# Kernel optimization log

Measured on AMD Instinct MI355X. Metric: run time of the kernel, lower is better.

## Reference

```python
import jax, jax.numpy as jnp
import numpy as np
import math

B, S, D, H, L, V = 2, 2048, 1024, 16, 2, 32000
HD = D // H          # head_dim = 64
FF = 4 * D           # ffn hidden = 4096
NEG_INF = -1e9


def setup_inputs() -> dict:
    key = jax.random.key(0)
    ks = jax.random.split(key, 12)
    w = lambda k, shape: jax.random.normal(k, shape, dtype=jnp.float32) * 0.02
    return {
        "tokens": jax.random.randint(ks[0], (B, S), 0, V),
        "tok_emb": w(ks[1], (V, D)),
        "pos_emb": w(ks[2], (S, D)),
        # torch nn.Linear weights are [out, in]; stacked over layers
        "wq": w(ks[3], (L, D, D)),
        "wk": w(ks[4], (L, D, D)),
        "wv": w(ks[5], (L, D, D)),
        "wo": w(ks[6], (L, D, D)),
        "w1": w(ks[7], (L, FF, D)),
        "w2": w(ks[8], (L, D, FF)),
        "ln1_g": jnp.ones((L, D)), "ln1_b": jnp.zeros((L, D)),
        "ln2_g": jnp.ones((L, D)), "ln2_b": jnp.zeros((L, D)),
        "lnf_g": jnp.ones((D,)), "lnf_b": jnp.zeros((D,)),
        "w_out": w(ks[9], (V, D)),
    }


def _layernorm(x, g, b):
    m = jnp.mean(x, axis=-1, keepdims=True)
    v = jnp.mean(jnp.square(x - m), axis=-1, keepdims=True)
    return (x - m) * jax.lax.rsqrt(v + 1e-5) * g + b


def _transformer(tokens, tok_emb, pos_emb, wq, wk, wv, wo, w1, w2,
                 ln1_g, ln1_b, ln2_g, ln2_b, lnf_g, lnf_b, w_out):
    s = tokens.shape[1]
    # causal additive mask [1,1,S,S]
    mask = jnp.where(jnp.tril(jnp.ones((s, s), dtype=bool)), 0.0, NEG_INF)[None, None]
    h = tok_emb[tokens] + pos_emb[None, :s]
    scale = 1.0 / math.sqrt(HD)
    for l in range(L):
        # pre-norm attention
        a_in = _layernorm(h, ln1_g[l], ln1_b[l])
        q = (a_in @ wq[l].T).reshape(B, s, H, HD)
        k = (a_in @ wk[l].T).reshape(B, s, H, HD)
        v = (a_in @ wv[l].T).reshape(B, s, H, HD)
        scores = jnp.einsum('bqhd,bkhd->bhqk', q, k) * scale + mask
        attn = jax.nn.softmax(scores.astype(jnp.float32), axis=-1).astype(h.dtype)
        o = jnp.einsum('bhqk,bkhd->bqhd', attn, v).reshape(B, s, D)
        h = h + o @ wo[l].T
        # pre-norm ReLU FFN
        f_in = _layernorm(h, ln2_g[l], ln2_b[l])
        h = h + jax.nn.relu(f_in @ w1[l].T) @ w2[l].T
    h = _layernorm(h, lnf_g, lnf_b)
    return h @ w_out.T  # [B,S,V]


def reference(tokens, tok_emb, pos_emb, wq, wk, wv, wo, w1, w2,
              ln1_g, ln1_b, ln2_g, ln2_b, lnf_g, lnf_b, w_out):
    return _transformer(tokens, tok_emb, pos_emb, wq, wk, wv, wo, w1, w2,
                        ln1_g, ln1_b, ln2_g, ln2_b, lnf_g, lnf_b, w_out)
```

## Files before the change

kernel.cpp:

```cpp
#include <hip/hip_runtime.h>

#define Bv 2
#define Sv 2048
#define Dv 1024
#define Hv 16
#define HDv 64
#define FFv 4096
#define Vv 32000

typedef short bf16x8 __attribute__((ext_vector_type(8)));
typedef float f32x4 __attribute__((ext_vector_type(4)));
typedef unsigned short us8 __attribute__((ext_vector_type(8)));
typedef unsigned short us4 __attribute__((ext_vector_type(4)));
typedef unsigned short u16;

__device__ __forceinline__ u16 f2bf(float f) {
  union { float f; unsigned u; } x; x.f = f;
  x.u += 0x7fffu + ((x.u >> 16) & 1u);
  return (u16)(x.u >> 16);
}
__device__ __forceinline__ u16 f2bf_rtz(float f) {
  union { float f; unsigned u; } x; x.f = f;
  return (u16)(x.u >> 16);
}

__device__ __forceinline__ void gld16(const void* g, void* l) {
  __builtin_amdgcn_global_load_lds(
      (const __attribute__((address_space(1))) unsigned*)g,
      (__attribute__((address_space(3))) unsigned*)l, 16, 0, 0);
}

__global__ __launch_bounds__(256) void k_embed(const int* __restrict__ tok,
    const float* __restrict__ te, const float* __restrict__ pe,
    float* __restrict__ h) {
  int row = blockIdx.x;
  int s = row & (Sv - 1);
  int t = tok[row];
  float4 va = ((const float4*)(te + (size_t)t * Dv))[threadIdx.x];
  float4 vb = ((const float4*)(pe + (size_t)s * Dv))[threadIdx.x];
  float4 o;
  o.x = va.x + vb.x; o.y = va.y + vb.y; o.z = va.z + vb.z; o.w = va.w + vb.w;
  ((float4*)(h + (size_t)row * Dv))[threadIdx.x] = o;
}

__global__ __launch_bounds__(256) void k_cvt(const float* __restrict__ x,
    u16* __restrict__ y, int n4) {
  int i = blockIdx.x * 256 + threadIdx.x;
  if (i >= n4) return;
  float4 v = ((const float4*)x)[i];
  us4 o = { f2bf(v.x), f2bf(v.y), f2bf(v.z), f2bf(v.w) };
  ((us4*)y)[i] = o;
}

__global__ __launch_bounds__(256) void k_ln(const float* __restrict__ x,
    const float* __restrict__ g, const float* __restrict__ bb,
    u16* __restrict__ y) {
  int row = blockIdx.x, t = threadIdx.x;
  float4 v = ((const float4*)(x + (size_t)row * Dv))[t];
  float s = v.x + v.y + v.z + v.w;
#pragma unroll
  for (int m = 32; m; m >>= 1) s += __shfl_xor(s, m, 64);
  __shared__ float red[4];
  if ((t & 63) == 0) red[t >> 6] = s;
  __syncthreads();
  float mean = (red[0] + red[1] + red[2] + red[3]) * (1.0f / Dv);
  __syncthreads();
  float dx = v.x - mean, dy = v.y - mean, dz = v.z - mean, dw = v.w - mean;
  float s2 = dx * dx + dy * dy + dz * dz + dw * dw;
#pragma unroll
  for (int m = 32; m; m >>= 1) s2 += __shfl_xor(s2, m, 64);
  if ((t & 63) == 0) red[t >> 6] = s2;
  __syncthreads();
  float var = (red[0] + red[1] + red[2] + red[3]) * (1.0f / Dv);
  float rstd = rsqrtf(var + 1e-5f);
  float4 gg = ((const float4*)g)[t];
  float4 be = ((const float4*)bb)[t];
  us4 o = { f2bf(dx * rstd * gg.x + be.x), f2bf(dy * rstd * gg.y + be.y),
            f2bf(dz * rstd * gg.z + be.z), f2bf(dw * rstd * gg.w + be.w) };
  ((us4*)(y + (size_t)row * Dv))[t] = o;
}

__device__ __forceinline__ void stage32(const u16* __restrict__ g, int ldK,
    u16* lds, int row_base, int kt, int lane) {
  int row = row_base + (lane >> 2);
  int slot = (lane & 3) ^ ((row >> 1) & 3);
  const u16* src = g + (size_t)row * ldK + (kt << 5) + (slot << 3);
  gld16(src, lds + (row_base << 5));
}
__device__ __forceinline__ bf16x8 ldfragA(const u16* lds, int row, int ks) {
  return *(const bf16x8*)((const char*)lds + row * 64 + ((ks ^ ((row >> 1) & 3)) << 4));
}

template <int EPI>
__global__ __launch_bounds__(512, 4) void k_gemm8(const u16* __restrict__ A,
    const u16* __restrict__ Bm, const float* __restrict__ res,
    float* __restrict__ Cf, u16* __restrict__ Cb, int M, int N, int K) {
  __shared__ u16 As[3][128 * 32];
  __shared__ u16 Bs[3][256 * 32];
  int TM = M >> 7, TN = N >> 8, nwg = TM * TN;
  int orig = blockIdx.x;
  int qd = nwg >> 3, rm = nwg & 7, xcd = orig & 7;
  int wg = (xcd < rm ? xcd * (qd + 1) : rm * (qd + 1) + (xcd - rm) * qd) + (orig >> 3);
  int bm = wg % TM, bn = wg / TM;
  int m0 = bm << 7, n0 = bn << 8;
  int lane = threadIdx.x & 63, wid = threadIdx.x >> 6;
  int wr = wid >> 2, wc = wid & 3;
  int NT = K >> 5;
  const u16* Ag = A + (size_t)m0 * K;
  const u16* Bg = Bm + (size_t)n0 * K;
  int frow = lane & 15, ks = lane >> 4;

  f32x4 acc[4][4] = {};
  bf16x8 af[4], bf[4];

#pragma unroll
  for (int tt = 0; tt < 2; tt++) {
    stage32(Ag, K, As[tt], wid * 16, tt, lane);
    stage32(Bg, K, Bs[tt], wid * 32, tt, lane);
    stage32(Bg, K, Bs[tt], wid * 32 + 16, tt, lane);
  }
  asm volatile("s_waitcnt vmcnt(3)" ::: "memory");
  __builtin_amdgcn_s_barrier();

  int p = 0;
  for (int t = 0; t < NT; t++) {
    int q = p + 2 >= 3 ? p - 1 : p + 2;
    if (t + 2 < NT) {
      stage32(Ag, K, As[q], wid * 16, t + 2, lane);
      stage32(Bg, K, Bs[q], wid * 32, t + 2, lane);
      stage32(Bg, K, Bs[q], wid * 32 + 16, t + 2, lane);
    }
    const u16* Ab = As[p];
    const u16* Bb = Bs[p];
#pragma unroll
    for (int f = 0; f < 4; f++) af[f] = ldfragA(Ab, wr * 64 + f * 16 + frow, ks);
#pragma unroll
    for (int n = 0; n < 4; n++) bf[n] = ldfragA(Bb, wc * 64 + n * 16 + frow, ks);
    __builtin_amdgcn_s_setprio(1);
#pragma unroll
    for (int f = 0; f < 4; f++)
#pragma unroll
      for (int n = 0; n < 4; n++)
        acc[f][n] = __builtin_amdgcn_mfma_f32_16x16x32_bf16(af[f], bf[n], acc[f][n], 0, 0, 0);
    __builtin_amdgcn_s_setprio(0);
    if (t + 2 < NT) { asm volatile("s_waitcnt vmcnt(3)" ::: "memory"); }
    else            { asm volatile("s_waitcnt vmcnt(0)" ::: "memory"); }
    __builtin_amdgcn_s_barrier();
    p = p + 1 >= 3 ? 0 : p + 1;
  }

#pragma unroll
  for (int f = 0; f < 4; f++) {
#pragma unroll
    for (int r = 0; r < 4; r++) {
      int row = m0 + wr * 64 + f * 16 + (lane >> 4) * 4 + r;
#pragma unroll
      for (int n = 0; n < 4; n++) {
        int col = n0 + wc * 64 + n * 16 + frow;
        float val = acc[f][n][r];
        size_t idx = (size_t)row * N + col;
        if constexpr (EPI == 1) { Cf[idx] = val + res[idx]; }
        else if constexpr (EPI == 0) { __builtin_nontemporal_store(val, &Cf[idx]); }
        else if constexpr (EPI == 2) { Cb[idx] = f2bf(val); }
        else { Cb[idx] = f2bf(fmaxf(val, 0.0f)); }
      }
    }
  }
}

template <int EPI>
__global__ __launch_bounds__(256, 4) void k_gemmn(const u16* __restrict__ A,
    const u16* __restrict__ Bm, const float* __restrict__ res,
    float* __restrict__ Cf, u16* __restrict__ Cb, int M, int N, int K) {
  __shared__ u16 As[3][64 * 32];
  __shared__ u16 Bs[3][128 * 32];
  int TM = M >> 6, TN = N >> 7, nwg = TM * TN;
  int orig = blockIdx.x;
  int qd = nwg >> 3, rm = nwg & 7, xcd = orig & 7;
  int wg = (xcd < rm ? xcd * (qd + 1) : rm * (qd + 1) + (xcd - rm) * qd) + (orig >> 3);
  int bm = wg % TM, bn = wg / TM;
  int m0 = bm << 6, n0 = bn << 7;
  int lane = threadIdx.x & 63, wid = threadIdx.x >> 6;
  int wr = wid >> 1, wc = wid & 1;
  int NT = K >> 5;
  const u16* Ag = A + (size_t)m0 * K;
  const u16* Bg = Bm + (size_t)n0 * K;
  int frow = lane & 15, ks = lane >> 4;

  f32x4 acc[2][4] = {};
  bf16x8 af[2], bf[4];

#pragma unroll
  for (int tt = 0; tt < 2; tt++) {
    stage32(Ag, K, As[tt], wid * 16, tt, lane);
    stage32(Bg, K, Bs[tt], wid * 32, tt, lane);
    stage32(Bg, K, Bs[tt], wid * 32 + 16, tt, lane);
  }
  asm volatile("s_waitcnt vmcnt(3)" ::: "memory");
  __builtin_amdgcn_s_barrier();

  int p = 0;
  for (int t = 0; t < NT; t++) {
    int q = p + 2 >= 3 ? p - 1 : p + 2;
    if (t + 2 < NT) {
      stage32(Ag, K, As[q], wid * 16, t + 2, lane);
      stage32(Bg, K, Bs[q], wid * 32, t + 2, lane);
      stage32(Bg, K, Bs[q], wid * 32 + 16, t + 2, lane);
    }
    const u16* Ab = As[p];
    const u16* Bb = Bs[p];
#pragma unroll
    for (int f = 0; f < 2; f++) af[f] = ldfragA(Ab, wr * 32 + f * 16 + frow, ks);
#pragma unroll
    for (int n = 0; n < 4; n++) bf[n] = ldfragA(Bb, wc * 64 + n * 16 + frow, ks);
    __builtin_amdgcn_s_setprio(1);
#pragma unroll
    for (int f = 0; f < 2; f++)
#pragma unroll
      for (int n = 0; n < 4; n++)
        acc[f][n] = __builtin_amdgcn_mfma_f32_16x16x32_bf16(af[f], bf[n], acc[f][n], 0, 0, 0);
    __builtin_amdgcn_s_setprio(0);
    if (t + 2 < NT) { asm volatile("s_waitcnt vmcnt(3)" ::: "memory"); }
    else            { asm volatile("s_waitcnt vmcnt(0)" ::: "memory"); }
    __builtin_amdgcn_s_barrier();
    p = p + 1 >= 3 ? 0 : p + 1;
  }

#pragma unroll
  for (int f = 0; f < 2; f++) {
#pragma unroll
    for (int r = 0; r < 4; r++) {
      int row = m0 + wr * 32 + f * 16 + (lane >> 4) * 4 + r;
#pragma unroll
      for (int n = 0; n < 4; n++) {
        int col = n0 + wc * 64 + n * 16 + frow;
        float val = acc[f][n][r];
        size_t idx = (size_t)row * N + col;
        if constexpr (EPI == 1) { Cf[idx] = val + res[idx]; }
        else if constexpr (EPI == 0) { __builtin_nontemporal_store(val, &Cf[idx]); }
        else if constexpr (EPI == 2) { Cb[idx] = f2bf(val); }
        else { Cb[idx] = f2bf(fmaxf(val, 0.0f)); }
      }
    }
  }
}

__global__ __launch_bounds__(256) void k_transpose(const u16* __restrict__ v,
    u16* __restrict__ vt, int stride) {
  int st = blockIdx.x & 31;
  int bh = blockIdx.x >> 5;
  int b = bh >> 4, hh = bh & 15;
  __shared__ u16 tile[64][72];
  int t = threadIdx.x;
  int rr = t >> 3, cc = (t & 7) << 3;
#pragma unroll
  for (int it = 0; it < 2; it++) {
    int r = rr + it * 32;
    us8 val = *(const us8*)(v + (size_t)(b * Sv + st * 64 + r) * stride + hh * HDv + cc);
    *(us8*)&tile[r][cc] = val;
  }
  __syncthreads();
#pragma unroll
  for (int it = 0; it < 2; it++) {
    int d = rr + it * 32;
    us8 val;
#pragma unroll
    for (int j = 0; j < 8; j++) val[j] = tile[cc + j][d];
    *(us8*)(vt + ((size_t)bh * HDv + d) * Sv + st * 64 + cc) = val;
  }
}

__global__ __launch_bounds__(64) void k_attn(const u16* __restrict__ qg,
    const u16* __restrict__ kg, const u16* __restrict__ vt,
    u16* __restrict__ og) {
  int bid = blockIdx.x;
  int qt = 15 - (bid >> 7);
  int bh = (bid >> 2) & 31;
  int strip = bid & 3;
  int b = bh >> 4, hh = bh & 15;
  int lane = threadIdx.x;
  int q0 = qt * 128 + strip * 32;
  __shared__ u16 plds[32 * 40];
  const int QS = 3 * Dv;
  const float sc2 = 0.18033688f;
  int qcol = lane & 15, g = lane >> 4;

  bf16x8 onesf;
#pragma unroll
  for (int j = 0; j < 8; j++) onesf[j] = (short)0x3F80;

  bf16x8 qf[2][2];
#pragma unroll
  for (int fm = 0; fm < 2; fm++)
#pragma unroll
    for (int dh = 0; dh < 2; dh++)
      qf[fm][dh] = *(const bf16x8*)(qg + (size_t)(b * Sv + q0 + fm * 16 + qcol) * QS
                                    + hh * HDv + dh * 32 + g * 8);

  f32x4 oacc[2][4] = {};
  f32x4 sacc[2] = {};
  int nfull = q0 >> 5;

  for (int kt = 0; kt <= nfull; kt++) {
    int k0 = kt * 32;
    bool diag = (kt == nfull);
    bf16x8 kf[2][2];
#pragma unroll
    for (int kn = 0; kn < 2; kn++)
#pragma unroll
      for (int dh = 0; dh < 2; dh++)
        kf[kn][dh] = *(const bf16x8*)(kg + (size_t)(b * Sv + k0 + kn * 16 + qcol) * QS
                                      + hh * HDv + dh * 32 + g * 8);
    f32x4 sa[2][2] = {};
#pragma unroll
    for (int dh = 0; dh < 2; dh++)
#pragma unroll
      for (int fm = 0; fm < 2; fm++)
#pragma unroll
        for (int kn = 0; kn < 2; kn++)
          sa[fm][kn] = __builtin_amdgcn_mfma_f32_16x16x32_bf16(kf[kn][dh], qf[fm][dh], sa[fm][kn], 0, 0, 0);

#pragma unroll
    for (int fm = 0; fm < 2; fm++) {
      int qrow = fm * 16 + qcol;
      float pv[2][4];
#pragma unroll
      for (int kn = 0; kn < 2; kn++)
#pragma unroll
        for (int r = 0; r < 4; r++) {
          float e = exp2f(sa[fm][kn][r] * sc2);
          if (diag && (kn * 16 + g * 4 + r) > qrow) e = 0.0f;
          pv[kn][r] = e;
        }
#pragma unroll
      for (int kn = 0; kn < 2; kn++) {
        us4 pk = { f2bf_rtz(pv[kn][0]), f2bf_rtz(pv[kn][1]),
                   f2bf_rtz(pv[kn][2]), f2bf_rtz(pv[kn][3]) };
        *(us4*)(plds + (fm * 16 + qcol) * 40 + kn * 16 + g * 4) = pk;
      }
    }
    bf16x8 pf[2];
#pragma unroll
    for (int fm = 0; fm < 2; fm++)
      pf[fm] = *(const bf16x8*)(plds + (fm * 16 + qcol) * 40 + g * 8);
    bf16x8 vf[4];
#pragma unroll
    for (int dn = 0; dn < 4; dn++)
      vf[dn] = *(const bf16x8*)(vt + ((size_t)bh * HDv + dn * 16 + qcol) * Sv
                                + k0 + g * 8);
#pragma unroll
    for (int fm = 0; fm < 2; fm++) {
      sacc[fm] = __builtin_amdgcn_mfma_f32_16x16x32_bf16(pf[fm], onesf, sacc[fm], 0, 0, 0);
#pragma unroll
      for (int dn = 0; dn < 4; dn++)
        oacc[fm][dn] = __builtin_amdgcn_mfma_f32_16x16x32_bf16(pf[fm], vf[dn], oacc[fm][dn], 0, 0, 0);
    }
  }

#pragma unroll
  for (int fm = 0; fm < 2; fm++)
#pragma unroll
    for (int r = 0; r < 4; r++) {
      float li = 1.0f / sacc[fm][r];
      int row = q0 + fm * 16 + g * 4 + r;
#pragma unroll
      for (int dn = 0; dn < 4; dn++)
        og[(size_t)(b * Sv + row) * Dv + hh * HDv + dn * 16 + qcol] =
            f2bf(oacc[fm][dn][r] * li);
    }
}

extern "C" void kernel_launch(void* const* d_in, const int* in_sizes, int n_in,
                              void* d_out, int out_size, void* d_ws, size_t ws_size,
                              hipStream_t stream) {
  const int*   tok  = (const int*)d_in[0];
  const float* te   = (const float*)d_in[1];
  const float* pe   = (const float*)d_in[2];
  const float* wq   = (const float*)d_in[3];
  const float* wk   = (const float*)d_in[4];
  const float* wvv  = (const float*)d_in[5];
  const float* wo   = (const float*)d_in[6];
  const float* w1   = (const float*)d_in[7];
  const float* w2   = (const float*)d_in[8];
  const float* ln1g = (const float*)d_in[9];
  const float* ln1b = (const float*)d_in[10];
  const float* ln2g = (const float*)d_in[11];
  const float* ln2b = (const float*)d_in[12];
  const float* lnfg = (const float*)d_in[13];
  const float* lnfb = (const float*)d_in[14];
  const float* wout = (const float*)d_in[15];
  float* out = (float*)d_out;

  char* p = (char*)d_ws;
  float* h  = (float*)p; p += (size_t)4096 * 1024 * 4;
  u16* a    = (u16*)p;   p += (size_t)4096 * 1024 * 2;
  u16* qkv  = (u16*)p;   p += (size_t)4096 * 3072 * 2;
  u16* vt   = (u16*)p;   p += (size_t)32 * 64 * 2048 * 2;
  u16* o    = (u16*)p;   p += (size_t)4096 * 1024 * 2;
  u16* f1   = (u16*)p;   p += (size_t)4096 * 4096 * 2;
  u16* wb   = (u16*)p;   p += (size_t)32000 * 1024 * 2;

  const int M = Bv * Sv;

  k_embed<<<M, 256, 0, stream>>>(tok, te, pe, h);
  for (int l = 0; l < 2; l++) {
    k_ln<<<M, 256, 0, stream>>>(h, ln1g + l * Dv, ln1b + l * Dv, a);
    k_cvt<<<1024, 256, 0, stream>>>(wq  + (size_t)l * Dv * Dv, wb,              (Dv * Dv) / 4);
    k_cvt<<<1024, 256, 0, stream>>>(wk  + (size_t)l * Dv * Dv, wb + Dv * Dv,    (Dv * Dv) / 4);
    k_cvt<<<1024, 256, 0, stream>>>(wvv + (size_t)l * Dv * Dv, wb + 2 * Dv * Dv,(Dv * Dv) / 4);
    k_gemm8<2><<<32 * 12, 512, 0, stream>>>(a, wb, nullptr, nullptr, qkv, M, 3 * Dv, Dv);
    k_transpose<<<1024, 256, 0, stream>>>(qkv + 2 * Dv, vt, 3 * Dv);
    k_attn<<<2048, 64, 0, stream>>>(qkv, qkv + Dv, vt, o);
    k_cvt<<<1024, 256, 0, stream>>>(wo + (size_t)l * Dv * Dv, wb, (Dv * Dv) / 4);
    k_gemmn<1><<<64 * 8, 256, 0, stream>>>(o, wb, h, h, nullptr, M, Dv, Dv);
    k_ln<<<M, 256, 0, stream>>>(h, ln2g + l * Dv, ln2b + l * Dv, a);
    k_cvt<<<4096, 256, 0, stream>>>(w1 + (size_t)l * FFv * Dv, wb, (FFv * Dv) / 4);
    k_gemm8<3><<<32 * 16, 512, 0, stream>>>(a, wb, nullptr, nullptr, f1, M, FFv, Dv);
    k_cvt<<<4096, 256, 0, stream>>>(w2 + (size_t)l * Dv * FFv, wb, (Dv * FFv) / 4);
    k_gemmn<1><<<64 * 8, 256, 0, stream>>>(f1, wb, h, h, nullptr, M, Dv, FFv);
  }
  k_ln<<<M, 256, 0, stream>>>(h, lnfg, lnfb, a);
  k_cvt<<<32000, 256, 0, stream>>>(wout, wb, (Vv * Dv) / 4);
  k_gemm8<0><<<32 * 125, 512, 0, stream>>>(a, wb, nullptr, out, nullptr, M, Vv, Dv);
}
```

Measured before the change: 932.0 us.

## Load GEMM B fragments directly from global into registers, merge QKV weight conversions

The GEMM kernels stop staging the weight (B) operand through LDS. Each wave now loads its own B fragments straight from global memory into double-buffered registers one k-tile ahead, while A stays in a three-stage LDS pipeline. This removes B LDS traffic and halves shared memory, but each B load is an uncoalesced 16-byte access per lane, and B data is no longer shared between the waves that need the same columns. Separately, the three Q/K/V weight conversion launches are merged into a single kernel.

```diff
diff --git a/kernel.cpp b/kernel.cpp
--- a/kernel.cpp
+++ b/kernel.cpp
@@ -52,6 +52,18 @@
   ((us4*)y)[i] = o;
 }
 
+__global__ __launch_bounds__(256) void k_cvt3(const float* __restrict__ a,
+    const float* __restrict__ b, const float* __restrict__ c,
+    u16* __restrict__ y, int n4each) {
+  int i = blockIdx.x * 256 + threadIdx.x;
+  int sel = i / n4each;
+  int j = i - sel * n4each;
+  const float* src = sel == 0 ? a : (sel == 1 ? b : c);
+  float4 v = ((const float4*)src)[j];
+  us4 o = { f2bf(v.x), f2bf(v.y), f2bf(v.z), f2bf(v.w) };
+  ((us4*)y)[i] = o;
+}
+
 __global__ __launch_bounds__(256) void k_ln(const float* __restrict__ x,
     const float* __restrict__ g, const float* __restrict__ bb,
     u16* __restrict__ y) {
@@ -91,12 +103,39 @@
   return *(const bf16x8*)((const char*)lds + row * 64 + ((ks ^ ((row >> 1) & 3)) << 4));
 }
 
+#define TILE8(T, CUR, NXT, P)                                                \
+  {                                                                          \
+    if ((T) + 1 < NT) {                                                      \
+      const u16* bp = Bgw + ((T) + 1) * 32;                                  \
+      _Pragma("unroll")                                                      \
+      for (int n = 0; n < 4; n++)                                            \
+        NXT[n] = *(const bf16x8*)(bp + (size_t)n * 16 * K);                  \
+    }                                                                        \
+    if ((T) + 2 < NT)                                                        \
+      stage32(Ag, K, As[(P) + 2 >= 3 ? (P) - 1 : (P) + 2], wid * 16,         \
+              (T) + 2, lane);                                                \
+    _Pragma("unroll")                                                        \
+    for (int f = 0; f < 4; f++)                                              \
+      af[f] = ldfragA(As[P], wr * 64 + f * 16 + frow, ks);                   \
+    __builtin_amdgcn_s_setprio(1);                                           \
+    _Pragma("unroll")                                                        \
+    for (int f = 0; f < 4; f++)                                              \
+      _Pragma("unroll")                                                      \
+      for (int n = 0; n < 4; n++)                                            \
+        acc[f][n] = __builtin_amdgcn_mfma_f32_16x16x32_bf16(af[f], CUR[n],   \
+                                                            acc[f][n],0,0,0);\
+    __builtin_amdgcn_s_setprio(0);                                           \
+    __builtin_amdgcn_sched_barrier(0);                                       \
+    if ((T) + 2 < NT) { asm volatile("s_waitcnt vmcnt(1)" ::: "memory"); }   \
+    else              { asm volatile("s_waitcnt vmcnt(0)" ::: "memory"); }   \
+    __builtin_amdgcn_s_barrier();                                            \
+  }
+
 template <int EPI>
 __global__ __launch_bounds__(512, 4) void k_gemm8(const u16* __restrict__ A,
     const u16* __restrict__ Bm, const float* __restrict__ res,
     float* __restrict__ Cf, u16* __restrict__ Cb, int M, int N, int K) {
   __shared__ u16 As[3][128 * 32];
-  __shared__ u16 Bs[3][256 * 32];
   int TM = M >> 7, TN = N >> 8, nwg = TM * TN;
   int orig = blockIdx.x;
   int qd = nwg >> 3, rm = nwg & 7, xcd = orig & 7;
@@ -107,46 +146,25 @@
   int wr = wid >> 2, wc = wid & 3;
   int NT = K >> 5;
   const u16* Ag = A + (size_t)m0 * K;
-  const u16* Bg = Bm + (size_t)n0 * K;
   int frow = lane & 15, ks = lane >> 4;
+  const u16* Bgw = Bm + (size_t)n0 * K + (size_t)(wc * 64 + frow) * K + ks * 8;
 
   f32x4 acc[4][4] = {};
-  bf16x8 af[4], bf[4];
-
-#pragma unroll
-  for (int tt = 0; tt < 2; tt++) {
-    stage32(Ag, K, As[tt], wid * 16, tt, lane);
-    stage32(Bg, K, Bs[tt], wid * 32, tt, lane);
-    stage32(Bg, K, Bs[tt], wid * 32 + 16, tt, lane);
-  }
-  asm volatile("s_waitcnt vmcnt(3)" ::: "memory");
+  bf16x8 af[4], bf0[4], bf1[4];
+
+#pragma unroll
+  for (int n = 0; n < 4; n++) bf0[n] = *(const bf16x8*)(Bgw + (size_t)n * 16 * K);
+  stage32(Ag, K, As[0], wid * 16, 0, lane);
+  stage32(Ag, K, As[1], wid * 16, 1, lane);
+  asm volatile("s_waitcnt vmcnt(1)" ::: "memory");
   __builtin_amdgcn_s_barrier();
 
   int p = 0;
-  for (int t = 0; t < NT; t++) {
-    int q = p + 2 >= 3 ? p - 1 : p + 2;
-    if (t + 2 < NT) {
-      stage32(Ag, K, As[q], wid * 16, t + 2, lane);
-      stage32(Bg, K, Bs[q], wid * 32, t + 2, lane);
-      stage32(Bg, K, Bs[q], wid * 32 + 16, t + 2, lane);
-    }
-    const u16* Ab = As[p];
-    const u16* Bb = Bs[p];
-#pragma unroll
-    for (int f = 0; f < 4; f++) af[f] = ldfragA(Ab, wr * 64 + f * 16 + frow, ks);
-#pragma unroll
-    for (int n = 0; n < 4; n++) bf[n] = ldfragA(Bb, wc * 64 + n * 16 + frow, ks);
-    __builtin_amdgcn_s_setprio(1);
-#pragma unroll
-    for (int f = 0; f < 4; f++)
-#pragma unroll
-      for (int n = 0; n < 4; n++)
-        acc[f][n] = __builtin_amdgcn_mfma_f32_16x16x32_bf16(af[f], bf[n], acc[f][n], 0, 0, 0);
-    __builtin_amdgcn_s_setprio(0);
-    if (t + 2 < NT) { asm volatile("s_waitcnt vmcnt(3)" ::: "memory"); }
-    else            { asm volatile("s_waitcnt vmcnt(0)" ::: "memory"); }
-    __builtin_amdgcn_s_barrier();
-    p = p + 1 >= 3 ? 0 : p + 1;
+  for (int t = 0; t < NT; t += 2) {
+    TILE8(t, bf0, bf1, p);
+    int p1 = p + 1 >= 3 ? 0 : p + 1;
+    TILE8(t + 1, bf1, bf0, p1);
+    p = p1 + 1 >= 3 ? 0 : p1 + 1;
   }
 
 #pragma unroll
@@ -168,12 +186,39 @@
   }
 }
 
+#define TILEN(T, CUR, NXT, P)                                                \
+  {                                                                          \
+    if ((T) + 1 < NT) {                                                      \
+      const u16* bp = Bgw + ((T) + 1) * 32;                                  \
+      _Pragma("unroll")                                                      \
+      for (int n = 0; n < 4; n++)                                            \
+        NXT[n] = *(const bf16x8*)(bp + (size_t)n * 16 * K);                  \
+    }                                                                        \
+    if ((T) + 2 < NT)                                                        \
+      stage32(Ag, K, As[(P) + 2 >= 3 ? (P) - 1 : (P) + 2], wid * 16,         \
+              (T) + 2, lane);                                                \
+    _Pragma("unroll")                                                        \
+    for (int f = 0; f < 2; f++)                                              \
+      af[f] = ldfragA(As[P], wr * 32 + f * 16 + frow, ks);                   \
+    __builtin_amdgcn_s_setprio(1);                                           \
+    _Pragma("unroll")                                                        \
+    for (int f = 0; f < 2; f++)                                              \
+      _Pragma("unroll")                                                      \
+      for (int n = 0; n < 4; n++)                                            \
+        acc[f][n] = __builtin_amdgcn_mfma_f32_16x16x32_bf16(af[f], CUR[n],   \
+                                                            acc[f][n],0,0,0);\
+    __builtin_amdgcn_s_setprio(0);                                           \
+    __builtin_amdgcn_sched_barrier(0);                                       \
+    if ((T) + 2 < NT) { asm volatile("s_waitcnt vmcnt(1)" ::: "memory"); }   \
+    else              { asm volatile("s_waitcnt vmcnt(0)" ::: "memory"); }   \
+    __builtin_amdgcn_s_barrier();                                            \
+  }
+
 template <int EPI>
 __global__ __launch_bounds__(256, 4) void k_gemmn(const u16* __restrict__ A,
     const u16* __restrict__ Bm, const float* __restrict__ res,
     float* __restrict__ Cf, u16* __restrict__ Cb, int M, int N, int K) {
   __shared__ u16 As[3][64 * 32];
-  __shared__ u16 Bs[3][128 * 32];
   int TM = M >> 6, TN = N >> 7, nwg = TM * TN;
   int orig = blockIdx.x;
   int qd = nwg >> 3, rm = nwg & 7, xcd = orig & 7;
@@ -184,46 +229,25 @@
   int wr = wid >> 1, wc = wid & 1;
   int NT = K >> 5;
   const u16* Ag = A + (size_t)m0 * K;
-  const u16* Bg = Bm + (size_t)n0 * K;
   int frow = lane & 15, ks = lane >> 4;
+  const u16* Bgw = Bm + (size_t)n0 * K + (size_t)(wc * 64 + frow) * K + ks * 8;
 
   f32x4 acc[2][4] = {};
-  bf16x8 af[2], bf[4];
-
-#pragma unroll
-  for (int tt = 0; tt < 2; tt++) {
-    stage32(Ag, K, As[tt], wid * 16, tt, lane);
-    stage32(Bg, K, Bs[tt], wid * 32, tt, lane);
-    stage32(Bg, K, Bs[tt], wid * 32 + 16, tt, lane);
-  }
-  asm volatile("s_waitcnt vmcnt(3)" ::: "memory");
+  bf16x8 af[2], bf0[4], bf1[4];
+
+#pragma unroll
+  for (int n = 0; n < 4; n++) bf0[n] = *(const bf16x8*)(Bgw + (size_t)n * 16 * K);
+  stage32(Ag, K, As[0], wid * 16, 0, lane);
+  stage32(Ag, K, As[1], wid * 16, 1, lane);
+  asm volatile("s_waitcnt vmcnt(1)" ::: "memory");
   __builtin_amdgcn_s_barrier();
 
   int p = 0;
-  for (int t = 0; t < NT; t++) {
-    int q = p + 2 >= 3 ? p - 1 : p + 2;
-    if (t + 2 < NT) {
-      stage32(Ag, K, As[q], wid * 16, t + 2, lane);
-      stage32(Bg, K, Bs[q], wid * 32, t + 2, lane);
-      stage32(Bg, K, Bs[q], wid * 32 + 16, t + 2, lane);
-    }
-    const u16* Ab = As[p];
-    const u16* Bb = Bs[p];
-#pragma unroll
-    for (int f = 0; f < 2; f++) af[f] = ldfragA(Ab, wr * 32 + f * 16 + frow, ks);
-#pragma unroll
-    for (int n = 0; n < 4; n++) bf[n] = ldfragA(Bb, wc * 64 + n * 16 + frow, ks);
-    __builtin_amdgcn_s_setprio(1);
-#pragma unroll
-    for (int f = 0; f < 2; f++)
-#pragma unroll
-      for (int n = 0; n < 4; n++)
-        acc[f][n] = __builtin_amdgcn_mfma_f32_16x16x32_bf16(af[f], bf[n], acc[f][n], 0, 0, 0);
-    __builtin_amdgcn_s_setprio(0);
-    if (t + 2 < NT) { asm volatile("s_waitcnt vmcnt(3)" ::: "memory"); }
-    else            { asm volatile("s_waitcnt vmcnt(0)" ::: "memory"); }
-    __builtin_amdgcn_s_barrier();
-    p = p + 1 >= 3 ? 0 : p + 1;
+  for (int t = 0; t < NT; t += 2) {
+    TILEN(t, bf0, bf1, p);
+    int p1 = p + 1 >= 3 ? 0 : p + 1;
+    TILEN(t + 1, bf1, bf0, p1);
+    p = p1 + 1 >= 3 ? 0 : p1 + 1;
   }
 
 #pragma unroll
@@ -405,9 +429,8 @@
   k_embed<<<M, 256, 0, stream>>>(tok, te, pe, h);
   for (int l = 0; l < 2; l++) {
     k_ln<<<M, 256, 0, stream>>>(h, ln1g + l * Dv, ln1b + l * Dv, a);
-    k_cvt<<<1024, 256, 0, stream>>>(wq  + (size_t)l * Dv * Dv, wb,              (Dv * Dv) / 4);
-    k_cvt<<<1024, 256, 0, stream>>>(wk  + (size_t)l * Dv * Dv, wb + Dv * Dv,    (Dv * Dv) / 4);
-    k_cvt<<<1024, 256, 0, stream>>>(wvv + (size_t)l * Dv * Dv, wb + 2 * Dv * Dv,(Dv * Dv) / 4);
+    k_cvt3<<<3072, 256, 0, stream>>>(wq + (size_t)l * Dv * Dv, wk + (size_t)l * Dv * Dv,
+                                     wvv + (size_t)l * Dv * Dv, wb, (Dv * Dv) / 4);
     k_gemm8<2><<<32 * 12, 512, 0, stream>>>(a, wb, nullptr, nullptr, qkv, M, 3 * Dv, Dv);
     k_transpose<<<1024, 256, 0, stream>>>(qkv + 2 * Dv, vt, 3 * Dv);
     k_attn<<<2048, 64, 0, stream>>>(qkv, qkv + Dv, vt, o);
```

After: 1.569 ms. 1.68x slower.
